# Kernel optimization log

Measured on AMD Instinct MI355X. Metric: run time of the kernel, lower is better.

The kernel has to match this reference:

```python
import jax, jax.numpy as jnp
import numpy as np

N_NODES = 100000
N_EDGES = 1600000
IN_CH = 128
OUT_CH = 64
HID = 2 * OUT_CH  # 128


def setup_inputs() -> dict:
    key = jax.random.key(0)
    ks = jax.random.split(key, 8)
    x = jax.random.normal(ks[0], (N_NODES, IN_CH), dtype=jnp.float32)
    edge_index = jax.random.randint(ks[1], (2, N_EDGES), 0, N_NODES, dtype=jnp.int64)

    def glorot(k, shape):
        return jax.random.normal(k, shape, dtype=jnp.float32) / jnp.sqrt(jnp.float32(shape[0]))

    W1 = glorot(ks[2], (IN_CH, HID))
    b1 = jax.random.normal(ks[3], (HID,), dtype=jnp.float32) * 0.01
    W_mu = glorot(ks[4], (HID, OUT_CH))
    b_mu = jax.random.normal(ks[5], (OUT_CH,), dtype=jnp.float32) * 0.01
    W_logstd = glorot(ks[6], (HID, OUT_CH))
    b_logstd = jax.random.normal(ks[7], (OUT_CH,), dtype=jnp.float32) * 0.01
    return {"x": x, "edge_index": edge_index, "W1": W1, "b1": b1,
            "W_mu": W_mu, "b_mu": b_mu, "W_logstd": W_logstd, "b_logstd": b_logstd}


def _gcn_norm(edge_index, n_nodes):
    # PyG GCNConv: add self-loops, symmetric normalization deg^{-1/2} A deg^{-1/2}
    loop = jnp.arange(n_nodes, dtype=edge_index.dtype)
    src = jnp.concatenate([edge_index[0], loop])  # [E+N]
    dst = jnp.concatenate([edge_index[1], loop])  # [E+N]
    deg = jax.ops.segment_sum(jnp.ones_like(dst, dtype=jnp.float32), dst,
                              num_segments=n_nodes)
    dinv = jnp.where(deg > 0, jax.lax.rsqrt(jnp.maximum(deg, 1.0)), 0.0)
    norm = dinv[src] * dinv[dst]  # [E+N]
    return src, dst, norm


def _gcn_conv(x, src, dst, norm, W, b, n_nodes):
    h = x @ W                                   # [N, out] linear first (small out dims)
    msg = h[src] * norm[:, None]                # [E+N, out] gather + scale
    out = jax.ops.segment_sum(msg, dst, num_segments=n_nodes)  # scatter-add
    return out + b


def reference(x, edge_index, W1, b1, W_mu, b_mu, W_logstd, b_logstd):
    n = x.shape[0]
    src, dst, norm = _gcn_norm(edge_index, n)  # same graph for all three layers
    h = jax.nn.relu(_gcn_conv(x, src, dst, norm, W1, b1, n))
    mu = _gcn_conv(h, src, dst, norm, W_mu, b_mu, n)
    logstd = _gcn_conv(h, src, dst, norm, W_logstd, b_logstd, n)
    return mu, logstd
```

## Files before the change

### kernel.cpp

```cpp
#include <hip/hip_runtime.h>
#include <stdint.h>

#define N_NODES 100000
#define N_EDGES 1600000
#define BSHIFT 9
#define NB 196
#define CAP_T 9216
#define CAPP 11264
#define NGB 782
#define NBB 782

typedef __attribute__((ext_vector_type(8))) short short8;
typedef __attribute__((ext_vector_type(4))) float f32x4;
typedef __attribute__((ext_vector_type(2))) float f32x2;
typedef __attribute__((ext_vector_type(4))) unsigned u32x4;
typedef __attribute__((ext_vector_type(2))) unsigned u32x2;
typedef __attribute__((ext_vector_type(4))) int i32x4;

static __device__ __forceinline__ unsigned short f2bf(float f){
  unsigned u = __float_as_uint(f);
  u += 0x7fffu + ((u >> 16) & 1u);
  return (unsigned short)(u >> 16);
}
static __device__ __forceinline__ unsigned pack2bf(float a, float b){
  return (unsigned)f2bf(a) | ((unsigned)f2bf(b) << 16);
}
static __device__ __forceinline__ void upk8(u32x2 r, f32x2 w, f32x2* acc){
  #pragma unroll
  for (int b = 0; b < 2; ++b){
    unsigned u = r[b];
    f32x2 p0, p1;
    p0.x = (float)(int)(signed char)(u);
    p0.y = (float)(int)(signed char)(u >> 8);
    p1.x = (float)(int)(signed char)(u >> 16);
    p1.y = (float)(int)(signed char)(u >> 24);
    acc[2*b]     = __builtin_elementwise_fma(w, p0, acc[2*b]);
    acc[2*b + 1] = __builtin_elementwise_fma(w, p1, acc[2*b + 1]);
  }
}

__global__ __launch_bounds__(256)
void k_init(const float* __restrict__ W1, const float* __restrict__ Wmu,
            const float* __restrict__ Wls, short8* __restrict__ img,
            unsigned* __restrict__ gcur, float* __restrict__ dsc1,
            float* __restrict__ dsc2, unsigned* __restrict__ csr2){
  int t = threadIdx.x;
  if (blockIdx.x == 16){
    if (t < NB) gcur[t] = t * CAP_T;
    if (t < 64) csr2[(size_t)NB*CAPP + t] = (unsigned)N_NODES;
    if (t == 0){ dsc1[N_NODES] = 0.f; dsc2[N_NODES] = 0.f; }
    return;
  }
  int gid = blockIdx.x*256 + t;
  int k = gid >> 11, slot = gid & 2047;
  int lane = slot & 63, ks = (slot >> 6) & 3, tt = slot >> 8;
  int c = tt*16 + (lane & 15);
  int kb = ks*32 + (lane >> 4)*8;
  short8 v;
  #pragma unroll
  for (int j = 0; j < 8; ++j){
    float f;
    if (k == 0) f = W1[(kb + j)*128 + c];
    else        f = (c < 64) ? Wmu[(kb + j)*64 + c] : Wls[(kb + j)*64 + (c - 64)];
    v[j] = (short)f2bf(f);
  }
  img[gid] = v;
}

template<bool AF32, bool MULDINV>
static __device__ __forceinline__
void gemm_body(const void* __restrict__ A_, const short8* __restrict__ img,
               signed char* __restrict__ out8, float* __restrict__ scale,
               const float* __restrict__ dinv, int M, short8* wf, int tid, int bid)
{
  #pragma unroll
  for (int s = 0; s < 8; ++s) wf[tid + 256*s] = img[tid + 256*s];
  __syncthreads();

  int wave = tid >> 6, lane = tid & 63;
  int rb = bid*128 + wave*32;
  int r0 = rb + (lane & 15);
  int r1 = r0 + 16;
  int ra0 = min(r0, M-1), ra1 = min(r1, M-1);
  int koff = (lane >> 4)*8;

  short8 a0[4], a1[4];
  if (AF32){
    const float* A = (const float*)A_;
    #pragma unroll
    for (int ks = 0; ks < 4; ++ks){
      const float* p0 = A + (size_t)ra0*128 + ks*32 + koff;
      const float* p1 = A + (size_t)ra1*128 + ks*32 + koff;
      f32x4 xa = *(const f32x4*)p0, xb = *(const f32x4*)(p0 + 4);
      f32x4 ya = *(const f32x4*)p1, yb = *(const f32x4*)(p1 + 4);
      short8 t0, t1;
      #pragma unroll
      for (int j = 0; j < 4; ++j){
        t0[j] = (short)f2bf(xa[j]); t0[j+4] = (short)f2bf(xb[j]);
        t1[j] = (short)f2bf(ya[j]); t1[j+4] = (short)f2bf(yb[j]);
      }
      a0[ks] = t0; a1[ks] = t1;
    }
  } else {
    const unsigned short* A = (const unsigned short*)A_;
    #pragma unroll
    for (int ks = 0; ks < 4; ++ks){
      a0[ks] = *(const short8*)(A + (size_t)ra0*128 + ks*32 + koff);
      a1[ks] = *(const short8*)(A + (size_t)ra1*128 + ks*32 + koff);
    }
  }

  f32x4 acc[2][8];
  #pragma unroll
  for (int t = 0; t < 8; ++t){ acc[0][t] = (f32x4)0.f; acc[1][t] = (f32x4)0.f; }

  #pragma unroll
  for (int t = 0; t < 8; ++t){
    #pragma unroll
    for (int ks = 0; ks < 4; ++ks){
      short8 b = wf[(t*4 + ks)*64 + lane];
      acc[0][t] = __builtin_amdgcn_mfma_f32_16x16x32_bf16(a0[ks], b, acc[0][t], 0, 0, 0);
      acc[1][t] = __builtin_amdgcn_mfma_f32_16x16x32_bf16(a1[ks], b, acc[1][t], 0, 0, 0);
    }
  }

  #pragma unroll
  for (int sub = 0; sub < 2; ++sub){
    #pragma unroll
    for (int j = 0; j < 4; ++j){
      float m = 0.f;
      #pragma unroll
      for (int t = 0; t < 8; ++t) m = fmaxf(m, fabsf(acc[sub][t][j]));
      #pragma unroll
      for (int off = 1; off < 16; off <<= 1) m = fmaxf(m, __shfl_xor(m, off));
      int r = rb + sub*16 + (lane >> 4)*4 + j;
      if (r < M){
        float inv = 127.f / fmaxf(m, 1e-20f);
        #pragma unroll
        for (int t = 0; t < 8; ++t){
          int q = __float2int_rn(acc[sub][t][j] * inv);
          q = max(-127, min(127, q));
          out8[(size_t)r*128 + t*16 + (lane & 15)] = (signed char)q;
        }
        if ((lane & 15) == 0)
          scale[r] = (MULDINV ? dinv[r] : 1.f) * m * (1.f/127.f);
      }
    }
  }
}

static __device__ __forceinline__
void binB_body(const int* __restrict__ ei, unsigned* __restrict__ gcur,
               unsigned* __restrict__ tmp, char* smem, int t, int bb)
{
  unsigned* cnt   = (unsigned*)smem;
  unsigned* gbase = (unsigned*)(smem + 784);
  unsigned* loff  = (unsigned*)(smem + 1568);
  unsigned* sc    = (unsigned*)(smem + 2368);
  unsigned* sen   = (unsigned*)(smem + 3392);
  unsigned* spos  = (unsigned*)(smem + 11584);

  for (int j = t; j < NB; j += 256) cnt[j] = 0u;
  __syncthreads();
  unsigned bk[8], rk[8], en[8];
  int e0 = bb*2048 + t*8;
  #pragma unroll
  for (int half = 0; half < 2; ++half){
    i32x4 sv, dv;
    bool any = (e0 + half*4) < N_EDGES;
    if (any){
      sv = *(const i32x4*)(ei + e0 + half*4);
      dv = *(const i32x4*)(ei + N_EDGES + e0 + half*4);
    }
    #pragma unroll
    for (int j = 0; j < 4; ++j){
      int q = half*4 + j;
      int e = e0 + q;
      bool ok = e < N_EDGES;
      unsigned d = ok ? (unsigned)dv[j] : 0u;
      unsigned s = ok ? (unsigned)sv[j] : 0u;
      ok = ok && d < N_NODES && s < N_NODES;
      bk[q] = ok ? (d >> BSHIFT) : 0xffffffffu;
      rk[q] = 0u; en[q] = 0u;
      if (ok){ rk[q] = atomicAdd(&cnt[bk[q]], 1u); en[q] = s | ((d & 511u) << 17); }
    }
  }
  __syncthreads();
  sc[t] = (t < NB) ? cnt[t] : 0u;
  __syncthreads();
  for (int off = 1; off < 256; off <<= 1){
    unsigned a = (t >= off) ? sc[t - off] : 0u;
    __syncthreads();
    sc[t] += a;
    __syncthreads();
  }
  if (t < NB){
    loff[t]  = sc[t] - cnt[t];
    gbase[t] = cnt[t] ? atomicAdd(&gcur[t], cnt[t]) : 0u;
  }
  __syncthreads();
  unsigned total = sc[NB - 1];
  #pragma unroll
  for (int j = 0; j < 8; ++j)
    if (bk[j] != 0xffffffffu){
      unsigned lp = loff[bk[j]] + rk[j];
      unsigned gp = gbase[bk[j]] + rk[j];
      sen[lp]  = en[j];
      spos[lp] = (gp < (bk[j] + 1u)*CAP_T) ? gp : 0xffffffffu;
    }
  __syncthreads();
  for (unsigned idx = t; idx < total; idx += 256){
    unsigned p = spos[idx];
    if (p != 0xffffffffu) tmp[p] = sen[idx];
  }
}

__global__ __launch_bounds__(256)
void k_gemm_bin(const float* __restrict__ x, const short8* __restrict__ img,
                signed char* __restrict__ out8, float* __restrict__ rmax,
                const int* __restrict__ ei, unsigned* __restrict__ gcur,
                unsigned* __restrict__ tmp)
{
  __shared__ char smem[32768];
  int t = threadIdx.x;
  if (blockIdx.x < NGB)
    gemm_body<true, false>(x, img, out8, rmax, nullptr, N_NODES, (short8*)smem, t, blockIdx.x);
  else
    binB_body(ei, gcur, tmp, smem, t, blockIdx.x - NGB);
}

__global__ __launch_bounds__(256)
void k_gemm2(const unsigned short* __restrict__ A, const short8* __restrict__ img,
             signed char* __restrict__ out8, float* __restrict__ dscale,
             const float* __restrict__ dinv)
{
  __shared__ short8 wf[2048];
  gemm_body<false, true>(A, img, out8, dscale, dinv, N_NODES, wf, threadIdx.x, blockIdx.x);
}

__global__ __launch_bounds__(256)
void k_binC(const unsigned* __restrict__ gcur, const unsigned* __restrict__ tmp,
            unsigned* __restrict__ csr2, unsigned* __restrict__ begdeg,
            float* __restrict__ dinv, float* __restrict__ dsc1){
  __shared__ unsigned cnt[512];
  __shared__ unsigned cur[512];
  __shared__ unsigned sc[512];
  int b = blockIdx.x, t = threadIdx.x;
  unsigned base_t = (unsigned)b * CAP_T;
  unsigned basep  = (unsigned)b * CAPP;
  unsigned sz = min(gcur[b] - base_t, (unsigned)CAP_T);
  cnt[t] = 0u; cnt[t + 256] = 0u;
  __syncthreads();
  for (unsigned idx = t; idx < sz; idx += 256)
    atomicAdd(&cnt[(tmp[base_t + idx] >> 17) & 511u], 1u);
  __syncthreads();
  unsigned c0 = cnt[t], c1 = cnt[t + 256];
  unsigned p0 = (c0 + 7u) & ~7u, p1 = (c1 + 7u) & ~7u;
  sc[t] = p0; sc[t + 256] = p1;
  __syncthreads();
  for (int off = 1; off < 512; off <<= 1){
    unsigned a0 = (t >= off)       ? sc[t - off]       : 0u;
    unsigned a1 = (t + 256 >= off) ? sc[t + 256 - off] : 0u;
    __syncthreads();
    sc[t] += a0; sc[t + 256] += a1;
    __syncthreads();
  }
  unsigned e0 = sc[t] - p0, e1 = sc[t + 256] - p1;
  cur[t] = e0; cur[t + 256] = e1;
  {
    int n0 = b*512 + t, n1 = n0 + 256;
    if (n0 < N_NODES){
      begdeg[n0] = (((basep + e0) >> 3) << 11) | min(c0, 2047u);
      float dv = rsqrtf((float)(c0 + 1u));
      dinv[n0] = dv;
      dsc1[n0] *= dv;
      for (unsigned k = c0; k < p0; ++k) csr2[basep + e0 + k] = (unsigned)N_NODES;
    }
    if (n1 < N_NODES){
      begdeg[n1] = (((basep + e1) >> 3) << 11) | min(c1, 2047u);
      float dv = rsqrtf((float)(c1 + 1u));
      dinv[n1] = dv;
      dsc1[n1] *= dv;
      for (unsigned k = c1; k < p1; ++k) csr2[basep + e1 + k] = (unsigned)N_NODES;
    }
  }
  __syncthreads();
  for (unsigned idx = t; idx < sz; idx += 256){
    unsigned en = tmp[base_t + idx];
    unsigned p = atomicAdd(&cur[(en >> 17) & 511u], 1u);
    if (p < (unsigned)CAPP) csr2[basep + p] = en & 0x1FFFFu;
  }
}

template<int MODE>
__global__ __launch_bounds__(256)
void k_agg(const signed char* __restrict__ hin, const unsigned* __restrict__ begdeg,
           const unsigned* __restrict__ csr2, const float* __restrict__ dinv,
           const float* __restrict__ dscale,
           const float* __restrict__ bias, const float* __restrict__ bias2,
           unsigned* __restrict__ out_bf, float* __restrict__ out_f)
{
  int i = blockIdx.x*4 + (threadIdx.x >> 6);
  int lane = threadIdx.x & 63;
  int slot = lane >> 4, c8 = lane & 15;
  float di = dinv[i];

  f32x2 acc2[4];
  #pragma unroll
  for (int j = 0; j < 4; ++j){ acc2[j].x = 0.f; acc2[j].y = 0.f; }
  {
    u32x2 sv = *(const u32x2*)(hin + (size_t)i*128 + c8*8);
    float ws = (slot == 0) ? di * dscale[i] : 0.f;
    f32x2 wsv; wsv.x = ws; wsv.y = ws;
    upk8(sv, wsv, acc2);
  }

  unsigned pk = begdeg[i];
  unsigned beg = (pk >> 11) << 3;
  int nit = ((int)(pk & 2047u) + 7) >> 3;

  const u32x2* ep = (const u32x2*)(csr2 + beg + 2*slot);
  u32x2 eA = ep[0];
  u32x2 eB = ep[4];
  float dsA0 = dscale[eA[0]], dsA1 = dscale[eA[1]];
  u32x2 rA0 = *(const u32x2*)(hin + (size_t)eA[0]*128 + c8*8);
  u32x2 rA1 = *(const u32x2*)(hin + (size_t)eA[1]*128 + c8*8);

  for (int it = 0; it < nit; ++it){
    u32x2 eC = ep[4*it + 8];
    float dsB0 = dscale[eB[0]], dsB1 = dscale[eB[1]];
    u32x2 rB0 = *(const u32x2*)(hin + (size_t)eB[0]*128 + c8*8);
    u32x2 rB1 = *(const u32x2*)(hin + (size_t)eB[1]*128 + c8*8);

    f32x2 w0; w0.x = di * dsA0; w0.y = w0.x;
    f32x2 w1; w1.x = di * dsA1; w1.y = w1.x;
    upk8(rA0, w0, acc2);
    upk8(rA1, w1, acc2);

    eA = eB; eB = eC; dsA0 = dsB0; dsA1 = dsB1; rA0 = rB0; rA1 = rB1;
  }

  #pragma unroll
  for (int j = 0; j < 4; ++j){
    acc2[j].x += __shfl_xor(acc2[j].x, 16);
    acc2[j].x += __shfl_xor(acc2[j].x, 32);
    acc2[j].y += __shfl_xor(acc2[j].y, 16);
    acc2[j].y += __shfl_xor(acc2[j].y, 32);
  }

  if (slot != 0) return;
  int c0 = c8*8;
  if (MODE == 0){
    u32x4 o;
    #pragma unroll
    for (int j = 0; j < 4; ++j){
      float lo = fmaxf(acc2[j].x + bias[c0 + 2*j],     0.f);
      float hi = fmaxf(acc2[j].y + bias[c0 + 2*j + 1], 0.f);
      o[j] = pack2bf(lo, hi);
    }
    *(u32x4*)(out_bf + (size_t)i*64 + c8*4) = o;
  } else {
    const float* bsrc = (c8 < 8) ? (bias + c0) : (bias2 + (c0 - 64));
    float* base = (c8 < 8) ? (out_f + (size_t)i*64 + c0)
                           : (out_f + (size_t)N_NODES*64 + (size_t)i*64 + (c0 - 64));
    f32x4 o0, o1;
    o0[0] = acc2[0].x + bsrc[0]; o0[1] = acc2[0].y + bsrc[1];
    o0[2] = acc2[1].x + bsrc[2]; o0[3] = acc2[1].y + bsrc[3];
    o1[0] = acc2[2].x + bsrc[4]; o1[1] = acc2[2].y + bsrc[5];
    o1[2] = acc2[3].x + bsrc[6]; o1[3] = acc2[3].y + bsrc[7];
    __builtin_nontemporal_store(o0, (f32x4*)base);
    __builtin_nontemporal_store(o1, (f32x4*)(base + 4));
  }
}


extern "C" void kernel_launch(void* const* d_in, const int* in_sizes, int n_in,
                              void* d_out, int out_size, void* d_ws, size_t ws_size,
                              hipStream_t stream)
{
  const float* x   = (const float*)d_in[0];
  const int*   ei  = (const int*)d_in[1];
  const float* W1  = (const float*)d_in[2];
  const float* b1  = (const float*)d_in[3];
  const float* Wmu = (const float*)d_in[4];
  const float* bmu = (const float*)d_in[5];
  const float* Wls = (const float*)d_in[6];
  const float* bls = (const float*)d_in[7];
  float* out = (float*)d_out;

  char* ws = (char*)d_ws;
  unsigned*    begdeg = (unsigned*)ws;  ws += 400128;
  float*       dinv   = (float*)ws;     ws += 400128;
  float*       dsc1   = (float*)ws;     ws += 400128;
  float*       dsc2   = (float*)ws;     ws += 400128;
  unsigned*    gcur   = (unsigned*)ws;  ws += 1024;
  short8*      imgW   = (short8*)ws;    ws += 65536;
  unsigned*    csr2   = (unsigned*)ws;  ws += (size_t)NB*CAPP*4 + 256;
  unsigned*    tmp    = (unsigned*)ws;  ws += (size_t)NB*CAP_T*4;
  signed char* bufA   = (signed char*)ws; ws += 12800256;
  if (ws_size < (size_t)(ws - (char*)d_ws)) return;
  unsigned* bufB = (unsigned*)d_out;

  k_init<<<17, 256, 0, stream>>>(W1, Wmu, Wls, imgW, gcur, dsc1, dsc2, csr2);
  k_gemm_bin<<<NGB + NBB, 256, 0, stream>>>(x, imgW, bufA, dsc1, ei, gcur, tmp);
  k_binC<<<NB, 256, 0, stream>>>(gcur, tmp, csr2, begdeg, dinv, dsc1);

  k_agg<0><<<N_NODES/4, 256, 0, stream>>>(bufA, begdeg, csr2, dinv, dsc1, b1, nullptr,
                                          bufB, nullptr);
  k_gemm2<<<NGB, 256, 0, stream>>>((unsigned short*)bufB, imgW + 2048, bufA, dsc2, dinv);
  k_agg<1><<<N_NODES/4, 256, 0, stream>>>(bufA, begdeg, csr2, dinv, dsc2, bmu, bls,
                                          nullptr, out);
}
```

Baseline: 185.1 us.

## Permute int8 feature layout for packed stores and deepen aggregation prefetch

The GEMM epilogue now packs eight int8 quantized values per lane into one 64-bit store instead of eight scattered byte stores. This puts features in a channel-permuted layout, so the second-layer weights, the layer-1 bias and the final output indexing are permuted to match. The aggregation kernel also gets a three-deep software prefetch pipeline for edge gathers and moves to 512-thread blocks handling 8 nodes each. Costs are extra register pressure from the deeper pipeline and strided scalar output stores in the final kernel.

```diff
diff --git a/kernel.cpp b/kernel.cpp
--- a/kernel.cpp
+++ b/kernel.cpp
@@ -39,15 +39,18 @@
   }
 }
 
+
 __global__ __launch_bounds__(256)
 void k_init(const float* __restrict__ W1, const float* __restrict__ Wmu,
-            const float* __restrict__ Wls, short8* __restrict__ img,
-            unsigned* __restrict__ gcur, float* __restrict__ dsc1,
-            float* __restrict__ dsc2, unsigned* __restrict__ csr2){
+            const float* __restrict__ Wls, const float* __restrict__ b1,
+            short8* __restrict__ img, unsigned* __restrict__ gcur,
+            float* __restrict__ dsc1, float* __restrict__ dsc2,
+            unsigned* __restrict__ csr2, float* __restrict__ bias1p){
   int t = threadIdx.x;
   if (blockIdx.x == 16){
     if (t < NB) gcur[t] = t * CAP_T;
-    if (t < 64) csr2[(size_t)NB*CAPP + t] = (unsigned)N_NODES;
+    if (t < 96) csr2[(size_t)NB*CAPP + t] = (unsigned)N_NODES;
+    if (t < 128) bias1p[t] = b1[((t & 7) << 4) | (t >> 3)];
     if (t == 0){ dsc1[N_NODES] = 0.f; dsc2[N_NODES] = 0.f; }
     return;
   }
@@ -60,8 +63,13 @@
   #pragma unroll
   for (int j = 0; j < 8; ++j){
     float f;
-    if (k == 0) f = W1[(kb + j)*128 + c];
-    else        f = (c < 64) ? Wmu[(kb + j)*64 + c] : Wls[(kb + j)*64 + (c - 64)];
+    if (k == 0){
+      f = W1[(kb + j)*128 + c];
+    } else {
+      int kk = kb + j;
+      int kch = ((kk & 7) << 4) | (kk >> 3);
+      f = (c < 64) ? Wmu[kch*64 + c] : Wls[kch*64 + (c - 64)];
+    }
     v[j] = (short)f2bf(f);
   }
   img[gid] = v;
@@ -136,12 +144,21 @@
       int r = rb + sub*16 + (lane >> 4)*4 + j;
       if (r < M){
         float inv = 127.f / fmaxf(m, 1e-20f);
+        unsigned d0 = 0u, d1 = 0u;
         #pragma unroll
-        for (int t = 0; t < 8; ++t){
+        for (int t = 0; t < 4; ++t){
           int q = __float2int_rn(acc[sub][t][j] * inv);
           q = max(-127, min(127, q));
-          out8[(size_t)r*128 + t*16 + (lane & 15)] = (signed char)q;
+          d0 |= ((unsigned)q & 255u) << (8*t);
         }
+        #pragma unroll
+        for (int t = 4; t < 8; ++t){
+          int q = __float2int_rn(acc[sub][t][j] * inv);
+          q = max(-127, min(127, q));
+          d1 |= ((unsigned)q & 255u) << (8*(t - 4));
+        }
+        u32x2 dv; dv[0] = d0; dv[1] = d1;
+        *(u32x2*)(out8 + (size_t)r*128 + (lane & 15)*8) = dv;
         if ((lane & 15) == 0)
           scale[r] = (MULDINV ? dinv[r] : 1.f) * m * (1.f/127.f);
       }
@@ -293,14 +310,14 @@
 }
 
 template<int MODE>
-__global__ __launch_bounds__(256)
+__global__ __launch_bounds__(512)
 void k_agg(const signed char* __restrict__ hin, const unsigned* __restrict__ begdeg,
            const unsigned* __restrict__ csr2, const float* __restrict__ dinv,
            const float* __restrict__ dscale,
            const float* __restrict__ bias, const float* __restrict__ bias2,
            unsigned* __restrict__ out_bf, float* __restrict__ out_f)
 {
-  int i = blockIdx.x*4 + (threadIdx.x >> 6);
+  int i = blockIdx.x*8 + (threadIdx.x >> 6);
   int lane = threadIdx.x & 63;
   int slot = lane >> 4, c8 = lane & 15;
   float di = dinv[i];
@@ -320,24 +337,31 @@
   int nit = ((int)(pk & 2047u) + 7) >> 3;
 
   const u32x2* ep = (const u32x2*)(csr2 + beg + 2*slot);
-  u32x2 eA = ep[0];
-  u32x2 eB = ep[4];
-  float dsA0 = dscale[eA[0]], dsA1 = dscale[eA[1]];
-  u32x2 rA0 = *(const u32x2*)(hin + (size_t)eA[0]*128 + c8*8);
-  u32x2 rA1 = *(const u32x2*)(hin + (size_t)eA[1]*128 + c8*8);
-
-  for (int it = 0; it < nit; ++it){
-    u32x2 eC = ep[4*it + 8];
-    float dsB0 = dscale[eB[0]], dsB1 = dscale[eB[1]];
-    u32x2 rB0 = *(const u32x2*)(hin + (size_t)eB[0]*128 + c8*8);
-    u32x2 rB1 = *(const u32x2*)(hin + (size_t)eB[1]*128 + c8*8);
-
-    f32x2 w0; w0.x = di * dsA0; w0.y = w0.x;
-    f32x2 w1; w1.x = di * dsA1; w1.y = w1.x;
-    upk8(rA0, w0, acc2);
-    upk8(rA1, w1, acc2);
-
-    eA = eB; eB = eC; dsA0 = dsB0; dsA1 = dsB1; rA0 = rB0; rA1 = rB1;
+  u32x2 e1 = ep[4], e2 = ep[8];
+  {
+    u32x2 e0 = ep[0];
+    float dsA0 = dscale[e0[0]], dsA1 = dscale[e0[1]];
+    u32x2 rA0 = *(const u32x2*)(hin + (size_t)e0[0]*128 + c8*8);
+    u32x2 rA1 = *(const u32x2*)(hin + (size_t)e0[1]*128 + c8*8);
+    float dsB0 = dscale[e1[0]], dsB1 = dscale[e1[1]];
+    u32x2 rB0 = *(const u32x2*)(hin + (size_t)e1[0]*128 + c8*8);
+    u32x2 rB1 = *(const u32x2*)(hin + (size_t)e1[1]*128 + c8*8);
+
+    for (int it = 0; it < nit; ++it){
+      u32x2 e3 = ep[4*it + 12];
+      float dsC0 = dscale[e2[0]], dsC1 = dscale[e2[1]];
+      u32x2 rC0 = *(const u32x2*)(hin + (size_t)e2[0]*128 + c8*8);
+      u32x2 rC1 = *(const u32x2*)(hin + (size_t)e2[1]*128 + c8*8);
+
+      f32x2 w0; w0.x = di * dsA0; w0.y = w0.x;
+      f32x2 w1; w1.x = di * dsA1; w1.y = w1.x;
+      upk8(rA0, w0, acc2);
+      upk8(rA1, w1, acc2);
+
+      e2 = e3;
+      dsA0 = dsB0; dsA1 = dsB1; rA0 = rB0; rA1 = rB1;
+      dsB0 = dsC0; dsB1 = dsC1; rB0 = rC0; rB1 = rC1;
+    }
   }
 
   #pragma unroll
@@ -349,8 +373,8 @@
   }
 
   if (slot != 0) return;
-  int c0 = c8*8;
   if (MODE == 0){
+    int c0 = c8*8;
     u32x4 o;
     #pragma unroll
     for (int j = 0; j < 4; ++j){
@@ -360,16 +384,15 @@
     }
     *(u32x4*)(out_bf + (size_t)i*64 + c8*4) = o;
   } else {
-    const float* bsrc = (c8 < 8) ? (bias + c0) : (bias2 + (c0 - 64));
-    float* base = (c8 < 8) ? (out_f + (size_t)i*64 + c0)
-                           : (out_f + (size_t)N_NODES*64 + (size_t)i*64 + (c0 - 64));
-    f32x4 o0, o1;
-    o0[0] = acc2[0].x + bsrc[0]; o0[1] = acc2[0].y + bsrc[1];
-    o0[2] = acc2[1].x + bsrc[2]; o0[3] = acc2[1].y + bsrc[3];
-    o1[0] = acc2[2].x + bsrc[4]; o1[1] = acc2[2].y + bsrc[5];
-    o1[2] = acc2[3].x + bsrc[6]; o1[3] = acc2[3].y + bsrc[7];
-    __builtin_nontemporal_store(o0, (f32x4*)base);
-    __builtin_nontemporal_store(o1, (f32x4*)(base + 4));
+    #pragma unroll
+    for (int j = 0; j < 4; ++j){
+      const float* bb = (j < 2) ? bias : bias2;
+      float* dst = (j < 2) ? (out_f + (size_t)i*64)
+                           : (out_f + (size_t)N_NODES*64 + (size_t)i*64);
+      int ch0 = (j & 1)*32 + c8;
+      __builtin_nontemporal_store(acc2[j].x + bb[ch0],      &dst[ch0]);
+      __builtin_nontemporal_store(acc2[j].y + bb[ch0 + 16], &dst[ch0 + 16]);
+    }
   }
 }
 
@@ -393,21 +416,22 @@
   float*       dinv   = (float*)ws;     ws += 400128;
   float*       dsc1   = (float*)ws;     ws += 400128;
   float*       dsc2   = (float*)ws;     ws += 400128;
+  float*       bias1p = (float*)ws;     ws += 512;
   unsigned*    gcur   = (unsigned*)ws;  ws += 1024;
   short8*      imgW   = (short8*)ws;    ws += 65536;
-  unsigned*    csr2   = (unsigned*)ws;  ws += (size_t)NB*CAPP*4 + 256;
+  unsigned*    csr2   = (unsigned*)ws;  ws += (size_t)NB*CAPP*4 + 512;
   unsigned*    tmp    = (unsigned*)ws;  ws += (size_t)NB*CAP_T*4;
   signed char* bufA   = (signed char*)ws; ws += 12800256;
   if (ws_size < (size_t)(ws - (char*)d_ws)) return;
   unsigned* bufB = (unsigned*)d_out;
 
-  k_init<<<17, 256, 0, stream>>>(W1, Wmu, Wls, imgW, gcur, dsc1, dsc2, csr2);
+  k_init<<<17, 256, 0, stream>>>(W1, Wmu, Wls, b1, imgW, gcur, dsc1, dsc2, csr2, bias1p);
   k_gemm_bin<<<NGB + NBB, 256, 0, stream>>>(x, imgW, bufA, dsc1, ei, gcur, tmp);
   k_binC<<<NB, 256, 0, stream>>>(gcur, tmp, csr2, begdeg, dinv, dsc1);
 
-  k_agg<0><<<N_NODES/4, 256, 0, stream>>>(bufA, begdeg, csr2, dinv, dsc1, b1, nullptr,
+  k_agg<0><<<N_NODES/8, 512, 0, stream>>>(bufA, begdeg, csr2, dinv, dsc1, bias1p, nullptr,
                                           bufB, nullptr);
   k_gemm2<<<NGB, 256, 0, stream>>>((unsigned short*)bufB, imgW + 2048, bufA, dsc2, dinv);
-  k_agg<1><<<N_NODES/4, 256, 0, stream>>>(bufA, begdeg, csr2, dinv, dsc2, bmu, bls,
+  k_agg<1><<<N_NODES/8, 512, 0, stream>>>(bufA, begdeg, csr2, dinv, dsc2, bmu, bls,
                                           nullptr, out);
 }
```

After: 190.9 us. 3.2% more time.
